# Kernel optimization log

Measured on AMD Instinct MI355X. Metric: run time of the kernel, lower is better.

## Reference

```python
import jax, jax.numpy as jnp
import numpy as np

B, S, HID, NH, K = 4, 1500, 1024, 16, 64
DH = HID // NH  # 64


def _rel_bias(pos_emb, length):
    # pos_emb: [2K+1, d]; Shaw-style relative position embedding lookup -> [S, S, d]
    kk = (pos_emb.shape[0] - 1) // 2
    idx = jnp.arange(length)
    dist = jnp.clip(idx[None, :] - idx[:, None], -kk, kk) + kk
    return pos_emb[dist]


def setup_inputs() -> dict:
    key = jax.random.key(0)
    ks = jax.random.split(key, 12)
    sq = 1.0 / np.sqrt(HID)
    inp = {
        "query": jax.random.normal(ks[0], (B, S, HID), jnp.float32),
        "key": jax.random.normal(ks[1], (B, S, HID), jnp.float32),
        "value": jax.random.normal(ks[2], (B, S, HID), jnp.float32),
        # per-head QKV projections stacked over heads: [NH, HID, DH]
        "Wq": jax.random.normal(ks[3], (NH, HID, DH), jnp.float32) * sq,
        "bq": jnp.zeros((NH, DH), jnp.float32),
        "Wk": jax.random.normal(ks[4], (NH, HID, DH), jnp.float32) * sq,
        "bk": jnp.zeros((NH, DH), jnp.float32),
        "Wv": jax.random.normal(ks[5], (NH, HID, DH), jnp.float32) * sq,
        "bv": jnp.zeros((NH, DH), jnp.float32),
        # relative position tables [2K+1, DH]
        "pos_k": jax.random.normal(ks[6], (2 * K + 1, DH), jnp.float32) * 0.1,
        "pos_v": jax.random.normal(ks[7], (2 * K + 1, DH), jnp.float32) * 0.1,
        # output projection
        "W_fc": jax.random.normal(ks[8], (HID, HID), jnp.float32) * sq,
        "b_fc": jnp.zeros((HID,), jnp.float32),
    }
    return inp


def reference(query, key, value, Wq, bq, Wk, bk, Wv, bv, pos_k, pos_v, W_fc, b_fc):
    seq = query.shape[1]
    k_bias = _rel_bias(pos_k, seq)  # [S, S, DH]
    v_bias = _rel_bias(pos_v, seq)  # [S, S, DH]

    # batched per-head projections: [B, NH, S, DH]
    q = jnp.einsum('bsh,nhd->bnsd', query, Wq) + bq[None, :, None, :]
    k = jnp.einsum('bsh,nhd->bnsd', key, Wk) + bk[None, :, None, :]
    v = jnp.einsum('bsh,nhd->bnsd', value, Wv) + bv[None, :, None, :]

    attn_1 = jnp.einsum('bnqd,bnkd->bnqk', q, k)
    attn_2 = jnp.einsum('bnqd,qkd->bnqk', q, k_bias)  # Shaw relative key bias
    scores = (attn_1 + attn_2) / jnp.sqrt(jnp.float32(DH))
    w = jax.nn.softmax(scores, axis=-1)  # [B, NH, S, S]

    values_1 = jnp.einsum('bnqk,bnkd->bnqd', w, v)
    values_2 = jnp.einsum('bnqk,qkd->bnqd', w, v_bias)  # Shaw relative value bias
    heads = values_1 + values_2  # [B, NH, S, DH]

    # concat heads in head order -> [B, S, HID]
    hidden = jnp.transpose(heads, (0, 2, 1, 3)).reshape(query.shape[0], seq, -1)
    return hidden @ W_fc + b_fc
```

## Files before the change

### kernel.cpp

```cpp
#include <hip/hip_runtime.h>
#include <stdint.h>

typedef unsigned short u16;
typedef __attribute__((ext_vector_type(8))) short bf16x8;
typedef __attribute__((ext_vector_type(4))) float f32x4;

#define MFMA16(a, b, c) __builtin_amdgcn_mfma_f32_16x16x32_bf16(a, b, c, 0, 0, 0)

__device__ __forceinline__ u16 f2bf(float x) {
  union { float f; uint32_t u; } v; v.f = x;
  uint32_t r = (v.u + 0x7FFFu + ((v.u >> 16) & 1u)) >> 16;
  return (u16)r;
}
__device__ __forceinline__ float bf2f(u16 h) {
  union { uint32_t u; float f; } v; v.u = ((uint32_t)h) << 16; return v.f;
}
__device__ __forceinline__ uint cvt_pk_bf16(float a, float b) {
  uint r;
  asm("v_cvt_pk_bf16_f32 %0, %1, %2" : "=v"(r) : "v"(a), "v"(b));
  return r;
}
__device__ __forceinline__ void gll16(const void* g, void* s) {
  __builtin_amdgcn_global_load_lds((const __attribute__((address_space(1))) unsigned int*)g,
                                   (__attribute__((address_space(3))) unsigned int*)s, 16, 0, 0);
}


__global__ __launch_bounds__(256) void pack_x_kernel(const float* __restrict__ q,
                                                     const float* __restrict__ k,
                                                     const float* __restrict__ v,
                                                     u16* __restrict__ X) {
  const float* src = blockIdx.z == 0 ? q : (blockIdx.z == 1 ? k : v);
  u16* dst = X + (size_t)blockIdx.z * (6016UL * 1024UL);
  size_t idx = (size_t)blockIdx.x * 1024 + (size_t)threadIdx.x * 4;
  float4 f = *(const float4*)(src + idx);
  uint2 o;
  o.x = cvt_pk_bf16(f.x, f.y);
  o.y = cvt_pk_bf16(f.z, f.w);
  *(uint2*)(dst + idx) = o;
}

__global__ __launch_bounds__(256) void pack_w_kernel(const float* __restrict__ Wq,
                                                     const float* __restrict__ Wk,
                                                     const float* __restrict__ Wv,
                                                     const float* __restrict__ Wfc,
                                                     const float* __restrict__ bq,
                                                     const float* __restrict__ bk,
                                                     const float* __restrict__ bv,
                                                     const float* __restrict__ posk,
                                                     const float* __restrict__ posv,
                                                     u16* __restrict__ Wt,
                                                     u16* __restrict__ Wfct,
                                                     float* __restrict__ biascat,
                                                     u16* __restrict__ poskbf,
                                                     u16* __restrict__ posvT) {
  __shared__ float tile[64][65];
  const int bi = blockIdx.x;
  if (bi == 1024) {
    for (int i = threadIdx.x; i < 1024; i += 256) {
      biascat[i] = bq[i]; biascat[1024 + i] = bk[i]; biascat[2048 + i] = bv[i];
    }
    for (int i = threadIdx.x; i < 144 * 64; i += 256) {
      int r = i >> 6;
      poskbf[i] = (r < 129) ? f2bf(posk[i]) : (u16)0;
    }
    const int d = threadIdx.x & 63, rr = threadIdx.x >> 6;
#pragma unroll
    for (int j = 0; j < 34; ++j) {
      const int r = rr * 34 + j;
      posvT[d * 136 + r] = (r < 129) ? f2bf(posv[(size_t)r * 64 + d]) : (u16)0;
    }
    return;
  }
  const int r = threadIdx.x >> 2, c0 = (threadIdx.x & 3) * 16;
  const float* src;
  u16* outp;
  if (bi < 768) {
    const int z = bi >> 8, rem = bi & 255, n = rem >> 4, h0 = (rem & 15) * 64;
    const float* W = z == 0 ? Wq : (z == 1 ? Wk : Wv);
    src = W + (size_t)n * 65536 + (size_t)(h0 + r) * 64 + c0;
    outp = Wt + (size_t)z * (1024UL * 1024UL) + (size_t)(n * 64 + r) * 1024 + h0 + c0;
  } else {
    const int t = bi - 768;
    const int i0 = (t & 15) * 64, o0 = (t >> 4) * 64;
    src = Wfc + (size_t)(i0 + r) * 1024 + o0 + c0;
    outp = Wfct + (size_t)(o0 + r) * 1024 + i0 + c0;
  }
#pragma unroll
  for (int j = 0; j < 16; j += 4) {
    float4 f = *(const float4*)(src + j);
    tile[r][c0 + j] = f.x; tile[r][c0 + j + 1] = f.y;
    tile[r][c0 + j + 2] = f.z; tile[r][c0 + j + 3] = f.w;
  }
  __syncthreads();
#pragma unroll
  for (int j = 0; j < 16; ++j) outp[j] = f2bf(tile[c0 + j][r]);
}

__global__ __launch_bounds__(256) void vtrans_kernel(const u16* __restrict__ qkv,
                                                     u16* __restrict__ Vt) {
  const size_t ZS = 4UL * 16 * 1536 * 64;
  __shared__ u16 t[64][72];
  const int bh = blockIdx.x & 63, s0 = (blockIdx.x >> 6) * 64;
  const u16* src = qkv + 2 * ZS + (size_t)bh * (1536UL * 64UL) + (size_t)s0 * 64;
  const int r = threadIdx.x >> 2, c0 = (threadIdx.x & 3) * 16;
  *(uint4*)&t[r][c0]     = *(const uint4*)(src + (size_t)r * 64 + c0);
  *(uint4*)&t[r][c0 + 8] = *(const uint4*)(src + (size_t)r * 64 + c0 + 8);
  __syncthreads();
  uint4 a, bvec;
  uint tmp[8];
#pragma unroll
  for (int j = 0; j < 8; ++j)
    tmp[j] = (uint)t[c0 + 2 * j][r] | ((uint)t[c0 + 2 * j + 1][r] << 16);
  a.x = tmp[0]; a.y = tmp[1]; a.z = tmp[2]; a.w = tmp[3];
  bvec.x = tmp[4]; bvec.y = tmp[5]; bvec.z = tmp[6]; bvec.w = tmp[7];
  u16* dst = Vt + (size_t)(bh * 64 + r) * 1536 + s0 + c0;
  *(uint4*)dst = a;
  *(uint4*)(dst + 8) = bvec;
}

__global__ __launch_bounds__(256) void gemm_bt_kernel(
    const u16* __restrict__ Abase, long aStride,
    const u16* __restrict__ Bbase, long bStride,
    const float* __restrict__ biasBase, long biasStride,
    u16* __restrict__ outBF, float* __restrict__ outF, int mode) {
  const int z = blockIdx.z;
  const u16* A = Abase + (size_t)z * aStride;
  const u16* Bt = Bbase + (size_t)z * bStride;
  const float* bias = biasBase + (size_t)z * biasStride;
  __shared__ u16 As[128 * 32];
  __shared__ u16 Bs[128 * 32];
  const int tid = threadIdx.x, w = tid >> 6, lane = tid & 63;
  const int quad = lane >> 4, l16 = lane & 15;
  const int wm = w >> 1, wn = w & 1;
  const int m0 = blockIdx.y * 128, n0 = blockIdx.x * 128;
  const int srow = w * 16 + (lane >> 2);
  const int scol = (lane & 3) * 8;
  const u16* gA0 = A + (size_t)(m0 + srow) * 1024 + scol;
  const u16* gA1 = gA0 + 64UL * 1024;
  const u16* gB0 = Bt + (size_t)(n0 + srow) * 1024 + scol;
  const u16* gB1 = gB0 + 64UL * 1024;
  u16* lA0 = As + (w * 16) * 32;
  u16* lA1 = As + (64 + w * 16) * 32;
  u16* lB0 = Bs + (w * 16) * 32;
  u16* lB1 = Bs + (64 + w * 16) * 32;

  f32x4 acc[4][4];
  const f32x4 zf = {0.f, 0.f, 0.f, 0.f};
#pragma unroll
  for (int a = 0; a < 4; ++a)
#pragma unroll
    for (int b = 0; b < 4; ++b) acc[a][b] = zf;

  for (int kt = 0; kt < 32; ++kt) {
    const int k0 = kt * 32;
    gll16(gA0 + k0, lA0);
    gll16(gA1 + k0, lA1);
    gll16(gB0 + k0, lB0);
    gll16(gB1 + k0, lB1);
    __syncthreads();
    bf16x8 af[4], bfr[4];
#pragma unroll
    for (int f = 0; f < 4; ++f) {
      af[f]  = *(const bf16x8*)(As + (wm * 64 + f * 16 + l16) * 32 + quad * 8);
      bfr[f] = *(const bf16x8*)(Bs + (wn * 64 + f * 16 + l16) * 32 + quad * 8);
    }
#pragma unroll
    for (int fm = 0; fm < 4; ++fm)
#pragma unroll
      for (int fn = 0; fn < 4; ++fn)
        acc[fm][fn] = MFMA16(af[fm], bfr[fn], acc[fm][fn]);
    __syncthreads();
  }

  if (mode == 0) {
    const float scale = (z == 0) ? 0.125f : 1.0f;
    u16* out = outBF + (size_t)z * (4UL * 16 * 1536 * 64);
#pragma unroll
    for (int fm = 0; fm < 4; ++fm) {
#pragma unroll
      for (int i = 0; i < 4; ++i) {
        const int m = m0 + wm * 64 + fm * 16 + quad * 4 + i;
        if (m >= 6000) continue;
        const int bb = m / 1500;
        const int s = m - bb * 1500;
#pragma unroll
        for (int fn = 0; fn < 4; ++fn) {
          const int n = n0 + wn * 64 + fn * 16 + l16;
          const float vv = (acc[fm][fn][i] + bias[n]) * scale;
          const int h = n >> 6, d = n & 63;
          out[((size_t)(bb * 16 + h) * 1536 + s) * 64 + d] = f2bf(vv);
        }
      }
    }
  } else {
#pragma unroll
    for (int fm = 0; fm < 4; ++fm) {
#pragma unroll
      for (int i = 0; i < 4; ++i) {
        const int m = m0 + wm * 64 + fm * 16 + quad * 4 + i;
        if (m >= 6000) continue;
#pragma unroll
        for (int fn = 0; fn < 4; ++fn) {
          const int n = n0 + wn * 64 + fn * 16 + l16;
          outF[(size_t)m * 1024 + n] = acc[fm][fn][i] + bias[n];
        }
      }
    }
  }
}

__global__ __launch_bounds__(256) void attn_kernel(const u16* __restrict__ qkv,
                                                   const u16* __restrict__ Vt,
                                                   const u16* __restrict__ poskbf,
                                                   const u16* __restrict__ posvT,
                                                   const float* __restrict__ posv,
                                                   u16* __restrict__ hidden) {
  const size_t ZS = 4UL * 16 * 1536 * 64;
  __shared__ u16 qp_s[64 * 136];
  __shared__ u16 pb_s[64 * 136];
  __shared__ u16 kbuf[2][2048];
  __shared__ u16 vbuf[2][2048];

  const int tid = threadIdx.x;
  const int w = tid >> 6, lane = tid & 63, quad = lane >> 4, l16 = lane & 15;
  const int bi = blockIdx.x;
  const int bh = bi & 63;
  const int q0 = (bi >> 6) * 64, qw0 = q0 + w * 16;
  const int b = bh >> 4;
  const size_t sb = (size_t)bh * (1536UL * 64UL);
  const u16* Qp = qkv + sb;
  const u16* Kp = qkv + ZS + sb;
  const u16* Vtb = Vt + (size_t)bh * (64UL * 1536UL);
  u16* qp_row = qp_s + (w * 16 + l16) * 136;
  u16* pb_row = pb_s + (w * 16 + l16) * 136;

  const int r8 = lane >> 3, c8 = lane & 7;
  const int vr = lane >> 2, vc = lane & 3;
  auto stageK = [&](int it, int buf) {
    const u16* src = Kp + (size_t)(it * 32 + w * 8 + r8) * 64 + ((c8 ^ r8) * 8);
    gll16(src, &kbuf[buf][w * 512]);
  };
  auto stageV = [&](int it, int buf) {
    const u16* src = Vtb + (size_t)(w * 16 + vr) * 1536 + it * 32 + ((vc ^ ((vr >> 1) & 3)) * 8);
    gll16(src, &vbuf[buf][w * 512]);
  };

  {
    uint* pz = (uint*)(pb_s + w * 16 * 136);
    for (int i = lane; i < 1088; i += 64) pz[i] = 0u;
  }

  stageK(0, 0);
  stageV(0, 0);

  const u16* qptr = Qp + (size_t)(qw0 + l16) * 64 + quad * 8;
  const bf16x8 qB0 = *(const bf16x8*)qptr;
  const bf16x8 qB1 = *(const bf16x8*)(qptr + 32);

  const f32x4 zf = {0.f, 0.f, 0.f, 0.f};
#pragma unroll
  for (int nf = 0; nf < 9; ++nf) {
    const u16* bp = poskbf + (size_t)(nf * 16 + l16) * 64 + quad * 8;
    bf16x8 b0 = *(const bf16x8*)bp;
    bf16x8 b1 = *(const bf16x8*)(bp + 32);
    f32x4 c = zf;
    c = MFMA16(qB0, b0, c);
    c = MFMA16(qB1, b1, c);
    const int col = nf * 16 + l16;
    if (col < 136) {
#pragma unroll
      for (int i = 0; i < 4; ++i)
        qp_s[(w * 16 + quad * 4 + i) * 136 + col] = f2bf(c[i]);
    }
  }
  __syncthreads();

  const float L2E = 1.44269504f;
  const float M8 = -8.0f * L2E;
  const float eLow  = __builtin_fmaf(bf2f(qp_row[0]), L2E, M8);
  const float eHigh = __builtin_fmaf(bf2f(qp_row[128]), L2E, M8);

  f32x4 accf[4];
#pragma unroll
  for (int dc = 0; dc < 4; ++dc) accf[dc] = zf;
  float sSimple = 0.f, sLowSave = 0.f, sDall = 0.f, sD0 = 0.f, sD128 = 0.f;

  const int itLowEnd = (qw0 >= 95) ? (((qw0 - 95) >> 5) + 1) : 0;
  const int itHigh0 = (qw0 + 110) >> 5;
  const int dEnd = itHigh0 < 46 ? itHigh0 : 46;

  const int kswz = (quad ^ (l16 & 7)) * 8;
  const int kswz4 = ((quad + 4) ^ (l16 & 7)) * 8;
  const int vpos = (quad ^ ((l16 >> 1) & 3)) * 8;
  const int laneLo = ((quad & 1) << 5) + l16;
  const bool cgHi = quad >= 2;

  for (int it = 0; it < 47; ++it) {
    const int cur = it & 1;
    if (it < 46) { stageK(it + 1, cur ^ 1); stageV(it + 1, cur ^ 1); }

    if (it == itLowEnd) sLowSave = sSimple;
    const int phase = (it < itLowEnd) ? 0 : ((it >= 46) ? 1 : ((it < dEnd) ? 1 : 2));

    const u16* kb = kbuf[cur];
    bf16x8 ka00 = *(const bf16x8*)(kb + l16 * 64 + kswz);
    bf16x8 ka01 = *(const bf16x8*)(kb + l16 * 64 + kswz4);
    bf16x8 ka10 = *(const bf16x8*)(kb + (16 + l16) * 64 + kswz);
    bf16x8 ka11 = *(const bf16x8*)(kb + (16 + l16) * 64 + kswz4);
    const u16* vbse = vbuf[cur];
    bf16x8 vb0 = *(const bf16x8*)(vbse + l16 * 32 + vpos);
    bf16x8 vb1 = *(const bf16x8*)(vbse + (16 + l16) * 32 + vpos);
    bf16x8 vb2 = *(const bf16x8*)(vbse + (32 + l16) * 32 + vpos);
    bf16x8 vb3 = *(const bf16x8*)(vbse + (48 + l16) * 32 + vpos);

    float qb[2][4];
    if (phase == 1) {
      const int base = it * 32 + 64 - qw0 - l16;
#pragma unroll
      for (int cg = 0; cg < 2; ++cg) {
#pragma unroll
        for (int i = 0; i < 4; ++i) {
          int delta = base + cg * 16 + quad * 4 + i;
          delta = delta < 0 ? 0 : (delta > 128 ? 128 : delta);
          qb[cg][i] = bf2f(qp_row[delta]);
        }
      }
    }

    f32x4 cc[2];
    cc[0] = zf; cc[1] = zf;
    cc[0] = MFMA16(ka00, qB0, cc[0]);
    cc[0] = MFMA16(ka01, qB1, cc[0]);
    cc[1] = MFMA16(ka10, qB0, cc[1]);
    cc[1] = MFMA16(ka11, qB1, cc[1]);

    float pvv[2][4];
    if (phase != 1) {
      const float eB = (phase == 0) ? eLow : eHigh;
#pragma unroll
      for (int cg = 0; cg < 2; ++cg) {
#pragma unroll
        for (int i = 0; i < 4; ++i) {
          float p = __builtin_amdgcn_exp2f(__builtin_fmaf(cc[cg][i], L2E, eB));
          sSimple += p; pvv[cg][i] = p;
        }
      }
    } else {
      const int kc0 = it * 32;
#pragma unroll
      for (int cg = 0; cg < 2; ++cg) {
        const int krow0 = kc0 + cg * 16 + quad * 4;
        const int dbase = krow0 + 64 - qw0 - l16;
#pragma unroll
        for (int i = 0; i < 4; ++i) {
          int delta = dbase + i;
          delta = delta < 0 ? 0 : (delta > 128 ? 128 : delta);
          const float t = cc[cg][i] + qb[cg][i];
          float p = __builtin_amdgcn_exp2f(__builtin_fmaf(t, L2E, M8));
          if (krow0 + i >= 1500) p = 0.f;
          sDall += p;
          sD0   += (delta == 0)   ? p : 0.f;
          sD128 += (delta == 128) ? p : 0.f;
          pvv[cg][i] = p;
        }
        const uint pk01 = cvt_pk_bf16(pvv[cg][0], pvv[cg][1]);
        const uint pk23 = cvt_pk_bf16(pvv[cg][2], pvv[cg][3]);
        const u16 hb[4] = {(u16)pk01, (u16)(pk01 >> 16), (u16)pk23, (u16)(pk23 >> 16)};
#pragma unroll
        for (int i = 0; i < 4; ++i) {
          int delta = dbase + i;
          delta = delta < 0 ? 0 : (delta > 128 ? 128 : delta);
          if ((delta != 0) & (delta != 128)) pb_row[delta] = hb[i];
        }
      }
    }

    const uint u00 = cvt_pk_bf16(pvv[0][0], pvv[0][1]);
    const uint u01 = cvt_pk_bf16(pvv[0][2], pvv[0][3]);
    const uint u10 = cvt_pk_bf16(pvv[1][0], pvv[1][1]);
    const uint u11 = cvt_pk_bf16(pvv[1][2], pvv[1][3]);
    const uint lo00 = __shfl(u00, laneLo),      lo01 = __shfl(u01, laneLo);
    const uint lo10 = __shfl(u10, laneLo),      lo11 = __shfl(u11, laneLo);
    const uint hi00 = __shfl(u00, laneLo + 16), hi01 = __shfl(u01, laneLo + 16);
    const uint hi10 = __shfl(u10, laneLo + 16), hi11 = __shfl(u11, laneLo + 16);
    union { uint u[4]; bf16x8 v; } pa;
    pa.u[0] = cgHi ? lo10 : lo00;
    pa.u[1] = cgHi ? lo11 : lo01;
    pa.u[2] = cgHi ? hi10 : hi00;
    pa.u[3] = cgHi ? hi11 : hi01;

    accf[0] = MFMA16(pa.v, vb0, accf[0]);
    accf[1] = MFMA16(pa.v, vb1, accf[1]);
    accf[2] = MFMA16(pa.v, vb2, accf[2]);
    accf[3] = MFMA16(pa.v, vb3, accf[3]);

    __syncthreads();
  }

  const float sLow = sLowSave;
  const float sHigh = sSimple - sLowSave;
  float lpart = sSimple + sDall;
  float clow = sLow + sD0;
  float chigh = sHigh + sD128;
#pragma unroll
  for (int m = 16; m <= 32; m <<= 1) {
    lpart += __shfl_xor(lpart, m);
    clow  += __shfl_xor(clow, m);
    chigh += __shfl_xor(chigh, m);
  }
  const float linv = 1.0f / lpart;

  f32x4 o2[4];
#pragma unroll
  for (int dc = 0; dc < 4; ++dc) o2[dc] = zf;
  const u16* pbr = pb_s + (w * 16 + l16) * 136;
#pragma unroll
  for (int kk = 0; kk < 4; ++kk) {
    bf16x8 pa2 = *(const bf16x8*)(pbr + kk * 32 + quad * 8);
#pragma unroll
    for (int dc = 0; dc < 4; ++dc) {
      bf16x8 vb2r = *(const bf16x8*)(posvT + (size_t)(dc * 16 + l16) * 136 + kk * 32 + quad * 8);
      o2[dc] = MFMA16(pa2, vb2r, o2[dc]);
    }
  }

  float li[4], cl[4], ch[4];
#pragma unroll
  for (int i = 0; i < 4; ++i) {
    const int srcl = quad * 4 + i;
    li[i] = __shfl(linv, srcl);
    cl[i] = __shfl(clow, srcl);
    ch[i] = __shfl(chigh, srcl);
  }

#pragma unroll
  for (int dc = 0; dc < 4; ++dc) {
    const int d = dc * 16 + l16;
    const float pv0 = posv[d], pv1 = posv[128 * 64 + d];
#pragma unroll
    for (int i = 0; i < 4; ++i) {
      const int qg = qw0 + quad * 4 + i;
      if (qg < 1500) {
        const float val = (accf[dc][i] + o2[dc][i] + cl[i] * pv0 + ch[i] * pv1) * li[i];
        hidden[((size_t)(b * 1500 + qg)) * 1024 + (bh & 15) * 64 + d] = f2bf(val);
      }
    }
  }
}

extern "C" void kernel_launch(void* const* d_in, const int* in_sizes, int n_in,
                              void* d_out, int out_size, void* d_ws, size_t ws_size,
                              hipStream_t stream) {
  const float* query = (const float*)d_in[0];
  const float* key   = (const float*)d_in[1];
  const float* value = (const float*)d_in[2];
  const float* Wq = (const float*)d_in[3];
  const float* bq = (const float*)d_in[4];
  const float* Wk = (const float*)d_in[5];
  const float* bk = (const float*)d_in[6];
  const float* Wv = (const float*)d_in[7];
  const float* bv = (const float*)d_in[8];
  const float* posk = (const float*)d_in[9];
  const float* posv = (const float*)d_in[10];
  const float* Wfc = (const float*)d_in[11];
  const float* bfc = (const float*)d_in[12];
  float* out = (float*)d_out;

  char* p = (char*)d_ws;
  u16* X = (u16*)p;        p += 3UL * 6016 * 1024 * 2;
  u16* Wt = (u16*)p;       p += 3UL * 1024 * 1024 * 2;
  u16* Wfct = (u16*)p;     p += 1024UL * 1024 * 2;
  u16* poskbf = (u16*)p;   p += 144UL * 64 * 2;
  u16* posvT = (u16*)p;    p += 64UL * 136 * 2;
  float* biascat = (float*)p; p += 3UL * 1024 * 4;
  u16* qkv = (u16*)p;      p += 3UL * 4 * 16 * 1536 * 64 * 2;
  u16* hidden = X;
  u16* Vt = X + 6291456;

  pack_x_kernel<<<dim3(6000, 1, 3), 256, 0, stream>>>(query, key, value, X);
  pack_w_kernel<<<dim3(1025), 256, 0, stream>>>(Wq, Wk, Wv, Wfc, bq, bk, bv, posk, posv,
                                                Wt, Wfct, biascat, poskbf, posvT);

  gemm_bt_kernel<<<dim3(8, 47, 3), 256, 0, stream>>>(
      X, 6016L * 1024, Wt, 1024L * 1024, biascat, 1024L, qkv, nullptr, 0);

  vtrans_kernel<<<dim3(1536), 256, 0, stream>>>(qkv, Vt);

  attn_kernel<<<dim3(1536), 256, 0, stream>>>(qkv, Vt, poskbf, posvT, posv, hidden);

  gemm_bt_kernel<<<dim3(8, 47, 1), 256, 0, stream>>>(
      hidden, 0L, Wfct, 0L, bfc, 0L, nullptr, out, 1);
}
```

Before: 382.0 us.

## Prefetch K/V tiles into registers directly and drop LDS staging barrier

The attention loop no longer stages K and V tiles into double-buffered shared memory with global_load_lds. Each wave now loads its own MFMA fragments straight from global memory into registers, one iteration ahead, and rotates them at the end of the iteration. This removes the per-iteration __syncthreads and the LDS buffers, and adds a launch-bounds occupancy hint of 4. In exchange, the four waves of a block each fetch the same K/V data from global/L2. The extra prefetch registers may also raise register pressure or cause spills under the occupancy bound.

```diff
diff --git a/kernel.cpp b/kernel.cpp
--- a/kernel.cpp
+++ b/kernel.cpp
@@ -210,17 +210,15 @@
   }
 }
 
-__global__ __launch_bounds__(256) void attn_kernel(const u16* __restrict__ qkv,
-                                                   const u16* __restrict__ Vt,
-                                                   const u16* __restrict__ poskbf,
-                                                   const u16* __restrict__ posvT,
-                                                   const float* __restrict__ posv,
-                                                   u16* __restrict__ hidden) {
+__global__ __launch_bounds__(256, 4) void attn_kernel(const u16* __restrict__ qkv,
+                                                      const u16* __restrict__ Vt,
+                                                      const u16* __restrict__ poskbf,
+                                                      const u16* __restrict__ posvT,
+                                                      const float* __restrict__ posv,
+                                                      u16* __restrict__ hidden) {
   const size_t ZS = 4UL * 16 * 1536 * 64;
   __shared__ u16 qp_s[64 * 136];
   __shared__ u16 pb_s[64 * 136];
-  __shared__ u16 kbuf[2][2048];
-  __shared__ u16 vbuf[2][2048];
 
   const int tid = threadIdx.x;
   const int w = tid >> 6, lane = tid & 63, quad = lane >> 4, l16 = lane & 15;
@@ -235,24 +233,10 @@
   u16* qp_row = qp_s + (w * 16 + l16) * 136;
   u16* pb_row = pb_s + (w * 16 + l16) * 136;
 
-  const int r8 = lane >> 3, c8 = lane & 7;
-  const int vr = lane >> 2, vc = lane & 3;
-  auto stageK = [&](int it, int buf) {
-    const u16* src = Kp + (size_t)(it * 32 + w * 8 + r8) * 64 + ((c8 ^ r8) * 8);
-    gll16(src, &kbuf[buf][w * 512]);
-  };
-  auto stageV = [&](int it, int buf) {
-    const u16* src = Vtb + (size_t)(w * 16 + vr) * 1536 + it * 32 + ((vc ^ ((vr >> 1) & 3)) * 8);
-    gll16(src, &vbuf[buf][w * 512]);
-  };
-
   {
     uint* pz = (uint*)(pb_s + w * 16 * 136);
     for (int i = lane; i < 1088; i += 64) pz[i] = 0u;
   }
-
-  stageK(0, 0);
-  stageV(0, 0);
 
   const u16* qptr = Qp + (size_t)(qw0 + l16) * 64 + quad * 8;
   const bf16x8 qB0 = *(const bf16x8*)qptr;
@@ -290,29 +274,35 @@
   const int itHigh0 = (qw0 + 110) >> 5;
   const int dEnd = itHigh0 < 46 ? itHigh0 : 46;
 
-  const int kswz = (quad ^ (l16 & 7)) * 8;
-  const int kswz4 = ((quad + 4) ^ (l16 & 7)) * 8;
-  const int vpos = (quad ^ ((l16 >> 1) & 3)) * 8;
   const int laneLo = ((quad & 1) << 5) + l16;
   const bool cgHi = quad >= 2;
 
+  const u16* kBase = Kp + (size_t)l16 * 64 + quad * 8;
+  const u16* vBase = Vtb + (size_t)l16 * 1536 + quad * 8;
+
+  bf16x8 ka00 = *(const bf16x8*)(kBase);
+  bf16x8 ka01 = *(const bf16x8*)(kBase + 32);
+  bf16x8 ka10 = *(const bf16x8*)(kBase + 1024);
+  bf16x8 ka11 = *(const bf16x8*)(kBase + 1056);
+  bf16x8 vb0 = *(const bf16x8*)(vBase);
+  bf16x8 vb1 = *(const bf16x8*)(vBase + 16 * 1536);
+  bf16x8 vb2 = *(const bf16x8*)(vBase + 32 * 1536);
+  bf16x8 vb3 = *(const bf16x8*)(vBase + 48 * 1536);
+
   for (int it = 0; it < 47; ++it) {
-    const int cur = it & 1;
-    if (it < 46) { stageK(it + 1, cur ^ 1); stageV(it + 1, cur ^ 1); }
+    const u16* kn = kBase + (size_t)(it + 1) * 2048;
+    bf16x8 nk00 = *(const bf16x8*)(kn);
+    bf16x8 nk01 = *(const bf16x8*)(kn + 32);
+    bf16x8 nk10 = *(const bf16x8*)(kn + 1024);
+    bf16x8 nk11 = *(const bf16x8*)(kn + 1056);
+    const u16* vn = vBase + (it + 1) * 32;
+    bf16x8 nv0 = *(const bf16x8*)(vn);
+    bf16x8 nv1 = *(const bf16x8*)(vn + 16 * 1536);
+    bf16x8 nv2 = *(const bf16x8*)(vn + 32 * 1536);
+    bf16x8 nv3 = *(const bf16x8*)(vn + 48 * 1536);
 
     if (it == itLowEnd) sLowSave = sSimple;
     const int phase = (it < itLowEnd) ? 0 : ((it >= 46) ? 1 : ((it < dEnd) ? 1 : 2));
-
-    const u16* kb = kbuf[cur];
-    bf16x8 ka00 = *(const bf16x8*)(kb + l16 * 64 + kswz);
-    bf16x8 ka01 = *(const bf16x8*)(kb + l16 * 64 + kswz4);
-    bf16x8 ka10 = *(const bf16x8*)(kb + (16 + l16) * 64 + kswz);
-    bf16x8 ka11 = *(const bf16x8*)(kb + (16 + l16) * 64 + kswz4);
-    const u16* vbse = vbuf[cur];
-    bf16x8 vb0 = *(const bf16x8*)(vbse + l16 * 32 + vpos);
-    bf16x8 vb1 = *(const bf16x8*)(vbse + (16 + l16) * 32 + vpos);
-    bf16x8 vb2 = *(const bf16x8*)(vbse + (32 + l16) * 32 + vpos);
-    bf16x8 vb3 = *(const bf16x8*)(vbse + (48 + l16) * 32 + vpos);
 
     float qb[2][4];
     if (phase == 1) {
@@ -395,7 +385,8 @@
     accf[2] = MFMA16(pa.v, vb2, accf[2]);
     accf[3] = MFMA16(pa.v, vb3, accf[3]);
 
-    __syncthreads();
+    ka00 = nk00; ka01 = nk01; ka10 = nk10; ka11 = nk11;
+    vb0 = nv0; vb1 = nv1; vb2 = nv2; vb3 = nv3;
   }
 
   const float sLow = sLowSave;
```

New measurement: 549.1 us. +43.8%, slower.
